# Performance work log

Measured on AMD Instinct MI355X. Metric: run time of the kernel, lower is better.

## Reference

```python
import jax, jax.numpy as jnp
import numpy as np

NUM_LEVELS = 4
RADIUS = 4
DISP_SCALE = 64.0  # disparity magnitude range for synthetic inputs


def build_corr_pyramid(full_corr, num_levels=NUM_LEVELS):
    """full_corr: (B, Wr, H, Wl). Avg-pool (k=2, s=2, ceil_mode) along Wr per level."""
    pyr = [full_corr]
    cur = full_corr
    for _ in range(1, num_levels):
        B, Wr, H, Wl = cur.shape
        n2 = (Wr // 2) * 2
        pooled = cur[:, :n2].reshape(B, Wr // 2, 2, H, Wl).mean(axis=2)
        if Wr % 2 == 1:
            # ceil_mode: trailing window clipped to a single element
            pooled = jnp.concatenate([pooled, cur[:, -1:]], axis=1)
        pyr.append(pooled)
        cur = pooled
    return pyr


def sample_corr_pyramid_bilinear(pyr, disp, radius=RADIUS):
    """pyr[l]: (B, Wr_l, H, Wl); disp: (B,1,H,Wl).
    Sample 1D-bilinearly along Wr at index (i_left - disp)/2^l + off, off in [-r, r].
    Returns (B, K*L, H, Wl), K = 2r+1.
    """
    B, _, H, Wl = pyr[0].shape
    K = 2 * radius + 1
    base = jnp.arange(Wl, dtype=disp.dtype).reshape(1, 1, 1, Wl)
    offs = jnp.arange(-radius, radius + 1, dtype=disp.dtype).reshape(1, K, 1, 1)
    bi = jnp.arange(B).reshape(B, 1, 1, 1)
    hi = jnp.arange(H).reshape(1, 1, H, 1)
    wi = jnp.arange(Wl).reshape(1, 1, 1, Wl)
    outs = []
    for l, corr in enumerate(pyr):
        Wr_l = corr.shape[1]
        idx_c = (base - disp) / (2.0 ** l)          # (B,1,H,Wl)
        idx = jnp.clip(idx_c + offs, 0.0, Wr_l - 1)  # (B,K,H,Wl)
        idx0 = jnp.clip(jnp.floor(idx), 0.0, Wr_l - 1)
        idx1 = jnp.clip(idx0 + 1.0, 0.0, Wr_l - 1)
        w1 = idx - idx0
        i0 = idx0.astype(jnp.int32)
        i1 = idx1.astype(jnp.int32)
        # fused gather+interp: no (B,K,Wr_l,H,Wl) expansion
        v0 = corr[bi, i0, hi, wi]  # (B,K,H,Wl)
        v1 = corr[bi, i1, hi, wi]
        outs.append((1.0 - w1) * v0 + w1 * v1)
    return jnp.concatenate(outs, axis=1)  # (B, K*L, H, Wl)


def setup_inputs() -> dict:
    key = jax.random.key(0)
    k1, k2 = jax.random.split(key)
    B, Wr, H, Wl = 4, 320, 240, 320
    full_corr = jax.random.normal(k1, (B, Wr, H, Wl), dtype=jnp.float32)
    disp = jax.random.uniform(k2, (B, 1, H, Wl), dtype=jnp.float32) * DISP_SCALE
    return {"full_corr": full_corr, "disp": disp}


def reference(full_corr, disp):
    pyr = build_corr_pyramid(full_corr, NUM_LEVELS)
    return sample_corr_pyramid_bilinear(pyr, disp, RADIUS)
```

## Files before the change

kernel.cpp:

```cpp
#include <hip/hip_runtime.h>

#define NB 4
#define WR 320
#define NH 240
#define WL 320
#define NK 9
#define TW 16
#define NTILES 20
#define NS 10
#define HP 12
#define SLOTS 152
#define NI 19
#define BANDF (SLOTS * 2 * TW)
#define BUFSZ (BANDF + 64)
#define RSTRIDE ((size_t)NH * WL)
#define NBLK (NB * NTILES * HP)
#define NXCD 8

typedef const __attribute__((address_space(1))) void* gas_t;
typedef __attribute__((address_space(3))) void* las_t;

__device__ __forceinline__ void gld16(const float* g, float* l) {
  __builtin_amdgcn_global_load_lds((gas_t)g, (las_t)l, 16, 0, 0);
}
__device__ __forceinline__ void gld4(const float* g, float* l) {
  __builtin_amdgcn_global_load_lds((gas_t)g, (las_t)l, 4, 0, 0);
}

template <int L>
__device__ __forceinline__ float pooledf(const float* p, int j, int sbase,
                                         int hc) {
  const int a = ((j << L) + sbase) * 32 + hc;
  float v = p[a];
#pragma unroll
  for (int t = 1; t < (1 << L); ++t) v += p[a + t * 32];
  return v;
}

template <int L>
__device__ __forceinline__ void run_level(const float* __restrict__ corr,
                                          const float* __restrict__ disp,
                                          float* __restrict__ out, float* lds,
                                          int b, int h0, int w0, int lane) {
  const int dsr = lane >> 3;
  const int sh = (lane >> 2) & 1;
  const int c4 = (lane & 3) << 2;
  const int kq2 = lane >> 5;
  const int hh = (lane >> 4) & 1;
  const int c = lane & 15;
  const int hc = hh * 16 + c;
  const int sbase = 96 - w0;
  const float sc = 1.0f / (float)(1 << L);
  const int Wm1 = (WR >> L) - 1;
  const size_t cb = (size_t)b * WR * RSTRIDE;

  auto stage = [&](int qs) {
    float* bb = lds + (qs & 1) * BUFSZ;
#pragma unroll
    for (int i = L; i < NI; i += 4) {
      int rr = w0 - 96 + 8 * i + dsr;
      rr = min(max(rr, 0), WR - 1);
      const float* src =
          corr + cb + ((size_t)rr * NH + (h0 + 2 * qs + sh)) * WL + w0 + c4;
      gld16(src, bb + i * 256);
    }
    if (L == 3) {
      const float* dsrc =
          disp + ((size_t)b * NH + (h0 + 2 * qs + ((lane >> 4) & 1))) * WL +
          w0 + (lane & 15);
      gld4(dsrc, bb + BANDF);
    }
  };

  stage(0);
  stage(1);

#pragma unroll
  for (int q = 0; q < NS; ++q) {
    if (q == 0 || q == NS - 1)
      asm volatile("s_waitcnt vmcnt(5)" ::: "memory");
    else
      asm volatile("s_waitcnt vmcnt(10)" ::: "memory");
    __builtin_amdgcn_s_barrier();
    __builtin_amdgcn_sched_barrier(0);

    const float* bp = lds + (q & 1) * BUFSZ;
    const float dsp = bp[BANDF + hc];
    const float fidx = ((float)(w0 + c) - dsp) * sc;
    const int hq = h0 + 2 * q + hh;

#pragma unroll
    for (int m = 0; m < 5; ++m) {
      const int kraw = kq2 + 2 * m;
      const int k = min(kraw, 8);
      const float idx =
          fminf(fmaxf(fidx + (float)(k - 4), 0.0f), (float)Wm1);
      const int i0 = (int)idx;
      const int i1 = min(i0 + 1, Wm1);
      const float w = idx - (float)i0;
      const float v0 = pooledf<L>(bp, i0, sbase, hc);
      const float v1 = pooledf<L>(bp, i1, sbase, hc);
      if (kraw < NK) {
        out[((size_t)(b * (4 * NK) + L * NK + k) * NH + hq) * WL + w0 + c] =
            sc * fmaf(w, v1 - v0, v0);
      }
    }

    asm volatile("" ::: "memory");
    __builtin_amdgcn_s_barrier();
    asm volatile("" ::: "memory");
    if (q + 2 < NS) stage(q + 2);
    asm volatile("" ::: "memory");
  }
}

extern "C" __global__ __launch_bounds__(256, 4) void corr_sample_kernel(
    const float* __restrict__ corr, const float* __restrict__ disp,
    float* __restrict__ out) {
  __shared__ float lds0[2 * BUFSZ];

  const int bid = ((int)blockIdx.x & (NXCD - 1)) * (NBLK / NXCD) +
                  ((int)blockIdx.x >> 3);
  const int tile = bid % NTILES;
  const int rest = bid / NTILES;
  const int hp = rest % HP;
  const int b = rest / HP;
  const int w0 = tile * TW;
  const int h0 = hp * (2 * NS);

  const int lane = (int)threadIdx.x & 63;
  const int wv = (int)threadIdx.x >> 6;

  switch (wv) {
    case 0: run_level<0>(corr, disp, out, lds0, b, h0, w0, lane); break;
    case 1: run_level<1>(corr, disp, out, lds0, b, h0, w0, lane); break;
    case 2: run_level<2>(corr, disp, out, lds0, b, h0, w0, lane); break;
    default: run_level<3>(corr, disp, out, lds0, b, h0, w0, lane); break;
  }
}

extern "C" void kernel_launch(void* const* d_in, const int* in_sizes, int n_in,
                              void* d_out, int out_size, void* d_ws,
                              size_t ws_size, hipStream_t stream) {
  const float* corr = (const float*)d_in[0];
  const float* disp = (const float*)d_in[1];
  float* out = (float*)d_out;
  corr_sample_kernel<<<NBLK, 256, 0, stream>>>(corr, disp, out);
}
```

Measured before the change: 45.42 us.

## Replace per-block double-buffered row loop with one row-pair per block

Each block now handles a single pair of rows (HH=2) instead of looping over 10 row-pairs with a double-buffered LDS pipeline. The block issues its loads once, waits on vmcnt(0) and a barrier, then samples. LDS per block is halved and launch bounds rise to 8 blocks per CU, so latency is hidden through occupancy rather than software pipelining. This launches ten times as many blocks, adding per-block launch and index overhead and removing intra-block load/compute overlap.

```diff
diff --git a/kernel.cpp b/kernel.cpp
--- a/kernel.cpp
+++ b/kernel.cpp
@@ -7,14 +7,13 @@
 #define NK 9
 #define TW 16
 #define NTILES 20
-#define NS 10
-#define HP 12
+#define HH 2
 #define SLOTS 152
 #define NI 19
-#define BANDF (SLOTS * 2 * TW)
-#define BUFSZ (BANDF + 64)
+#define DISPOFF (SLOTS * HH * TW)
+#define LDSF (DISPOFF + 64)
 #define RSTRIDE ((size_t)NH * WL)
-#define NBLK (NB * NTILES * HP)
+#define NBLK (NB * NTILES * (NH / HH))
 #define NXCD 8
 
 typedef const __attribute__((address_space(1))) void* gas_t;
@@ -38,104 +37,82 @@
 }
 
 template <int L>
-__device__ __forceinline__ void run_level(const float* __restrict__ corr,
-                                          const float* __restrict__ disp,
-                                          float* __restrict__ out, float* lds,
-                                          int b, int h0, int w0, int lane) {
-  const int dsr = lane >> 3;
-  const int sh = (lane >> 2) & 1;
-  const int c4 = (lane & 3) << 2;
-  const int kq2 = lane >> 5;
+__device__ __forceinline__ void sample_level(const float* __restrict__ lds,
+                                             int lane, int b, int h0, int w0,
+                                             float* __restrict__ out) {
+  const int kpar = lane >> 5;
   const int hh = (lane >> 4) & 1;
   const int c = lane & 15;
   const int hc = hh * 16 + c;
   const int sbase = 96 - w0;
   const float sc = 1.0f / (float)(1 << L);
   const int Wm1 = (WR >> L) - 1;
-  const size_t cb = (size_t)b * WR * RSTRIDE;
 
-  auto stage = [&](int qs) {
-    float* bb = lds + (qs & 1) * BUFSZ;
-#pragma unroll
-    for (int i = L; i < NI; i += 4) {
-      int rr = w0 - 96 + 8 * i + dsr;
-      rr = min(max(rr, 0), WR - 1);
-      const float* src =
-          corr + cb + ((size_t)rr * NH + (h0 + 2 * qs + sh)) * WL + w0 + c4;
-      gld16(src, bb + i * 256);
-    }
-    if (L == 3) {
-      const float* dsrc =
-          disp + ((size_t)b * NH + (h0 + 2 * qs + ((lane >> 4) & 1))) * WL +
-          w0 + (lane & 15);
-      gld4(dsrc, bb + BANDF);
-    }
-  };
-
-  stage(0);
-  stage(1);
+  const float dsp = lds[DISPOFF + hc];
+  const float fidx = ((float)(w0 + c) - dsp) * sc;
 
 #pragma unroll
-  for (int q = 0; q < NS; ++q) {
-    if (q == 0 || q == NS - 1)
-      asm volatile("s_waitcnt vmcnt(5)" ::: "memory");
-    else
-      asm volatile("s_waitcnt vmcnt(10)" ::: "memory");
-    __builtin_amdgcn_s_barrier();
-    __builtin_amdgcn_sched_barrier(0);
-
-    const float* bp = lds + (q & 1) * BUFSZ;
-    const float dsp = bp[BANDF + hc];
-    const float fidx = ((float)(w0 + c) - dsp) * sc;
-    const int hq = h0 + 2 * q + hh;
-
-#pragma unroll
-    for (int m = 0; m < 5; ++m) {
-      const int kraw = kq2 + 2 * m;
-      const int k = min(kraw, 8);
-      const float idx =
-          fminf(fmaxf(fidx + (float)(k - 4), 0.0f), (float)Wm1);
-      const int i0 = (int)idx;
-      const int i1 = min(i0 + 1, Wm1);
-      const float w = idx - (float)i0;
-      const float v0 = pooledf<L>(bp, i0, sbase, hc);
-      const float v1 = pooledf<L>(bp, i1, sbase, hc);
-      if (kraw < NK) {
-        out[((size_t)(b * (4 * NK) + L * NK + k) * NH + hq) * WL + w0 + c] =
-            sc * fmaf(w, v1 - v0, v0);
-      }
+  for (int m = 0; m < 5; ++m) {
+    const int kraw = kpar + 2 * m;
+    const int k = min(kraw, 8);
+    const float idx = fminf(fmaxf(fidx + (float)(k - 4), 0.0f), (float)Wm1);
+    const int i0 = (int)idx;
+    const int i1 = min(i0 + 1, Wm1);
+    const float w = idx - (float)i0;
+    const float v0 = pooledf<L>(lds, i0, sbase, hc);
+    const float v1 = pooledf<L>(lds, i1, sbase, hc);
+    if (kraw < NK) {
+      out[((size_t)(b * (4 * NK) + L * NK + k) * NH + (h0 + hh)) * WL + w0 +
+          c] = sc * fmaf(w, v1 - v0, v0);
     }
-
-    asm volatile("" ::: "memory");
-    __builtin_amdgcn_s_barrier();
-    asm volatile("" ::: "memory");
-    if (q + 2 < NS) stage(q + 2);
-    asm volatile("" ::: "memory");
   }
 }
 
-extern "C" __global__ __launch_bounds__(256, 4) void corr_sample_kernel(
+extern "C" __global__ __launch_bounds__(256, 8) void corr_sample_kernel(
     const float* __restrict__ corr, const float* __restrict__ disp,
     float* __restrict__ out) {
-  __shared__ float lds0[2 * BUFSZ];
+  __shared__ float lds0[LDSF];
 
   const int bid = ((int)blockIdx.x & (NXCD - 1)) * (NBLK / NXCD) +
                   ((int)blockIdx.x >> 3);
   const int tile = bid % NTILES;
   const int rest = bid / NTILES;
-  const int hp = rest % HP;
-  const int b = rest / HP;
+  const int hp = rest % (NH / HH);
+  const int b = rest / (NH / HH);
   const int w0 = tile * TW;
-  const int h0 = hp * (2 * NS);
+  const int h0 = hp * HH;
 
-  const int lane = (int)threadIdx.x & 63;
-  const int wv = (int)threadIdx.x >> 6;
+  const int tid = (int)threadIdx.x;
+  const int lane = tid & 63;
+  const int wv = tid >> 6;
+
+  {
+    const int ds = lane >> 3;
+    const int sh = (lane >> 2) & 1;
+    const int c4 = (lane & 3) << 2;
+    const size_t cb = (size_t)b * WR * RSTRIDE;
+    for (int g = wv; g < NI; g += 4) {
+      int rr = w0 - 96 + 8 * g + ds;
+      rr = min(max(rr, 0), WR - 1);
+      const float* src =
+          corr + cb + ((size_t)rr * NH + (h0 + sh)) * WL + w0 + c4;
+      gld16(src, &lds0[g * 256]);
+    }
+    if (wv == 3) {
+      const float* dsrc = disp + ((size_t)b * NH + (h0 + ((lane >> 4) & 1))) * WL +
+                          w0 + (lane & 15);
+      gld4(dsrc, &lds0[DISPOFF]);
+    }
+  }
+
+  asm volatile("s_waitcnt vmcnt(0)" ::: "memory");
+  __syncthreads();
 
   switch (wv) {
-    case 0: run_level<0>(corr, disp, out, lds0, b, h0, w0, lane); break;
-    case 1: run_level<1>(corr, disp, out, lds0, b, h0, w0, lane); break;
-    case 2: run_level<2>(corr, disp, out, lds0, b, h0, w0, lane); break;
-    default: run_level<3>(corr, disp, out, lds0, b, h0, w0, lane); break;
+    case 0: sample_level<0>(lds0, lane, b, h0, w0, out); break;
+    case 1: sample_level<1>(lds0, lane, b, h0, w0, out); break;
+    case 2: sample_level<2>(lds0, lane, b, h0, w0, out); break;
+    default: sample_level<3>(lds0, lane, b, h0, w0, out); break;
   }
 }
 
```

Measured after the change: 41.60 us (median of 2 runs). -8.4%, faster.
